# Performance work log

Hardware: AMD Instinct MI355X
Metric: run time of the kernel (lower is better)

## Reference

```python
import jax, jax.numpy as jnp
import numpy as np

N, E, G = 10000, 160000, 64
NODE_DIM, HID = 128, 256


def _edge_conv(x, src, dst, w1, b1, w2, b2):
    # gather endpoints: x_i = target features, x_j = source features (PyG source_to_target)
    x_i = x[dst]                              # [E, C]
    x_j = x[src]                              # [E, C]
    m = jnp.concatenate([x_i, x_j - x_i], axis=-1)  # [E, 2C]
    m = jax.nn.relu(m @ w1 + b1) @ w2 + b2          # [E, H]
    out = jax.ops.segment_max(m, dst, num_segments=N)  # scatter-max per target node
    return out  # nodes with no in-edges get -inf; subsequent relu maps them to 0 (matches PyG fill 0 + relu)


def setup_inputs() -> dict:
    key = jax.random.key(0)
    ks = jax.random.split(key, 20)
    x = jax.random.normal(ks[0], (N, NODE_DIM), dtype=jnp.float32)
    edge_index = jax.random.randint(ks[1], (2, E), 0, N)
    batch = jnp.sort(jax.random.randint(ks[2], (N,), 0, G))
    s = 0.05
    inp = {"x": x, "edge_index": edge_index, "batch": batch}
    dims = [(2 * NODE_DIM, HID), (2 * HID, HID), (2 * HID, HID)]
    for li, (din, dout) in enumerate(dims):
        inp[f"c{li}_w1"] = jax.random.normal(ks[3 + 4 * li], (din, dout), jnp.float32) * s
        inp[f"c{li}_b1"] = jnp.zeros((dout,), jnp.float32)
        inp[f"c{li}_w2"] = jax.random.normal(ks[4 + 4 * li], (dout, dout), jnp.float32) * s
        inp[f"c{li}_b2"] = jnp.zeros((dout,), jnp.float32)
    inp["cl_w1"] = jax.random.normal(ks[15], (2 * HID, HID), jnp.float32) * s
    inp["cl_b1"] = jnp.zeros((HID,), jnp.float32)
    inp["cl_w2"] = jax.random.normal(ks[16], (HID, 64), jnp.float32) * s
    inp["cl_b2"] = jnp.zeros((64,), jnp.float32)
    inp["cl_w3"] = jax.random.normal(ks[17], (64, 1), jnp.float32) * s
    inp["cl_b3"] = jnp.zeros((1,), jnp.float32)
    return inp


def reference(x, edge_index, batch,
              c0_w1, c0_b1, c0_w2, c0_b2,
              c1_w1, c1_b1, c1_w2, c1_b2,
              c2_w1, c2_b1, c2_w2, c2_b2,
              cl_w1, cl_b1, cl_w2, cl_b2, cl_w3, cl_b3):
    src, dst = edge_index[0], edge_index[1]
    for (w1, b1, w2, b2) in [(c0_w1, c0_b1, c0_w2, c0_b2),
                             (c1_w1, c1_b1, c1_w2, c1_b2),
                             (c2_w1, c2_b1, c2_w2, c2_b2)]:
        x = jax.nn.relu(_edge_conv(x, src, dst, w1, b1, w2, b2))
    # global mean / max pool per graph
    sums = jax.ops.segment_sum(x, batch, num_segments=G)
    counts = jax.ops.segment_sum(jnp.ones((x.shape[0], 1), x.dtype), batch, num_segments=G)
    x_mean = sums / jnp.maximum(counts, 1.0)
    x_max = jax.ops.segment_max(x, batch, num_segments=G)
    x_max = jnp.where(counts > 0, x_max, 0.0)
    h = jnp.concatenate([x_mean, x_max], axis=1)  # [G, 2H]
    h = jax.nn.relu(h @ cl_w1 + cl_b1)            # dropout is eval-mode identity
    h = jax.nn.relu(h @ cl_w2 + cl_b2)
    out = (h @ cl_w3 + cl_b3).squeeze(-1)         # [G]
    return out
```

## Files before the change

kernel.cpp:

```cpp
#include <hip/hip_runtime.h>


#define NN 10000
#define NE 160000
#define NG 64
#define NP 10048
#define EB 64
#define TPB 5
#define NBLK 500

typedef __attribute__((ext_vector_type(8))) _Float16 f16x8;
typedef __attribute__((ext_vector_type(4))) _Float16 f16x4;
typedef __attribute__((ext_vector_type(4))) float f32x4;

#define LGKM_BARRIER() asm volatile("s_waitcnt lgkmcnt(0)\n\ts_barrier" ::: "memory")

__global__ void hist_kernel(const int* __restrict__ dstI, int* __restrict__ hist) {
    int i = blockIdx.x * blockDim.x + threadIdx.x;
    if (i < NE) atomicAdd(&hist[dstI[i]], 1);
}

__global__ void scan_kernel(const int* __restrict__ hist, int* __restrict__ cursor) {
    __shared__ int sums[256];
    const int t = threadIdx.x;
    const int per = (NN + 255) / 256;
    const int lo = t * per, hi = (lo + per < NN) ? lo + per : NN;
    int s = 0;
    for (int i = lo; i < hi; ++i) s += hist[i];
    sums[t] = s;
    __syncthreads();
    for (int ofs = 1; ofs < 256; ofs <<= 1) {
        int add = (t >= ofs) ? sums[t - ofs] : 0;
        __syncthreads();
        sums[t] += add;
        __syncthreads();
    }
    int run = sums[t] - s;
    for (int i = lo; i < hi; ++i) {
        int h = hist[i];
        cursor[i] = run;
        run += h;
    }
}

__global__ void scatter_kernel(const int* __restrict__ srcI, const int* __restrict__ dstI,
                               int* __restrict__ cursor,
                               int* __restrict__ se2, int* __restrict__ de2) {
    int i = blockIdx.x * blockDim.x + threadIdx.x;
    if (i < NE) {
        int d = dstI[i];
        int p = atomicAdd(&cursor[d], 1);
        se2[p] = srcI[i];
        de2[p] = d;
    }
}

__global__ void prep_weights(const float* __restrict__ w1, const float* __restrict__ w2, int C,
                             _Float16* __restrict__ WcT, _Float16* __restrict__ w2T) {
    int total1 = 512 * C;
    int total = total1 + 256 * 256;
    for (int i = blockIdx.x * blockDim.x + threadIdx.x; i < total; i += gridDim.x * blockDim.x) {
        if (i < total1) {
            int n = i / C, k = i - n * C;
            float v = (n < 256) ? (w1[k * 256 + n] - w1[(C + k) * 256 + n])
                                : w1[(C + k) * 256 + (n - 256)];
            WcT[n * C + k] = (_Float16)v;
        } else {
            int j = i - total1;
            int n = j >> 8, k = j & 255;
            w2T[n * 256 + k] = (_Float16)w2[k * 256 + n];
        }
    }
}

template <int C>
__global__ __launch_bounds__(256, 2) void node_gemm(
    const float* __restrict__ xf, const _Float16* __restrict__ WT,
    const float* __restrict__ b1, _Float16* __restrict__ Afh, _Float16* __restrict__ Bh) {
    const int wave = threadIdx.x >> 6, lane = threadIdx.x & 63;
    const int lrow = lane & 15, lk = (lane >> 4) * 8;
    const int r0 = blockIdx.x * 64;
    const int c0 = blockIdx.y * 256 + wave * 64;

    f32x4 acc[4][4] = {};
#pragma unroll
    for (int kk = 0; kk < C; kk += 32) {
        f16x8 ah[4];
#pragma unroll
        for (int m = 0; m < 4; ++m) {
            int rc = r0 + m * 16 + lrow;
            if (rc > NN - 1) rc = NN - 1;
            const float* xp = xf + (size_t)rc * C + kk + lk;
            const float4 v0 = *(const float4*)(xp);
            const float4 v1 = *(const float4*)(xp + 4);
            f16x8 a;
            a[0] = (_Float16)v0.x; a[1] = (_Float16)v0.y;
            a[2] = (_Float16)v0.z; a[3] = (_Float16)v0.w;
            a[4] = (_Float16)v1.x; a[5] = (_Float16)v1.y;
            a[6] = (_Float16)v1.z; a[7] = (_Float16)v1.w;
            ah[m] = a;
        }
#pragma unroll
        for (int t = 0; t < 4; ++t) {
            f16x8 bh = *(const f16x8*)(WT + (size_t)(c0 + t * 16 + lrow) * C + kk + lk);
#pragma unroll
            for (int m = 0; m < 4; ++m)
                acc[m][t] = __builtin_amdgcn_mfma_f32_16x16x32_f16(ah[m], bh, acc[m][t], 0, 0, 0);
        }
    }
    if (blockIdx.y == 0) {
#pragma unroll
        for (int t = 0; t < 4; ++t) {
            const int col = c0 + t * 16 + lrow;
            const float bias = b1[col];
#pragma unroll
            for (int m = 0; m < 4; ++m)
#pragma unroll
                for (int j = 0; j < 4; ++j) {
                    const int row = r0 + m * 16 + (lane >> 4) * 4 + j;
                    Afh[(size_t)row * 256 + col] = (_Float16)(acc[m][t][j] + bias);
                }
        }
    } else {
#pragma unroll
        for (int t = 0; t < 4; ++t) {
            const int col = c0 - 256 + t * 16 + lrow;
#pragma unroll
            for (int m = 0; m < 4; ++m)
#pragma unroll
                for (int j = 0; j < 4; ++j) {
                    const int row = r0 + m * 16 + (lane >> 4) * 4 + j;
                    Bh[(size_t)row * 256 + col] = (_Float16)acc[m][t][j];
                }
        }
    }
}

__global__ __launch_bounds__(512, 2) void edge_gemm(
    const _Float16* __restrict__ Afh, const _Float16* __restrict__ Bh,
    const int* __restrict__ se2, const int* __restrict__ de2,
    const _Float16* __restrict__ w2T,
    const float* __restrict__ b2, float* __restrict__ y) {
    __shared__ _Float16 hh[2 * EB * 256];
    const int tid = threadIdx.x;
    const int wave = tid >> 6, lane = tid & 63;
    const int lrow = lane & 15, lk = (lane >> 4) * 8;

    const int orig = blockIdx.x;
    const int xcd = orig & 7, pos = orig >> 3;
    const int qq = NBLK >> 3, rr = NBLK & 7;
    const int bid = (xcd < rr ? xcd * (qq + 1) : rr * (qq + 1) + (xcd - rr) * qq) + pos;
    const int t0 = bid * TPB;

    const _Float16* wbase = w2T + (size_t)(wave * 32 + lrow) * 256 + lk;

    f16x4 av[8], bv[8];

    auto stage_issue = [&](int tile) {
        int se[8], de[8];
#pragma unroll
        for (int i = 0; i < 8; ++i) {
            const int e = tile * EB + wave * 8 + i;
            se[i] = se2[e];
            de[i] = de2[e];
        }
#pragma unroll
        for (int i = 0; i < 8; ++i) {
            bv[i] = *(const f16x4*)(Bh + (size_t)se[i] * 256 + lane * 4);
            av[i] = *(const f16x4*)(Afh + (size_t)de[i] * 256 + lane * 4);
        }
    };
    auto stage_write = [&](int buf) {
#pragma unroll
        for (int i = 0; i < 8; ++i) {
            const int el = wave * 8 + i;
            const int row = ((el >> 2) & 3) * 16 + (el >> 4) * 4 + (el & 3);
            f16x4 h = av[i] + bv[i];
#pragma unroll
            for (int k = 0; k < 4; ++k) h[k] = h[k] > (_Float16)0.f ? h[k] : (_Float16)0.f;
            *(f16x4*)(&hh[buf * (EB * 256) + ((row * 256 + lane * 4) ^ ((row & 15) << 3))]) = h;
        }
    };

    stage_issue(t0);
    stage_write(0);
    LGKM_BARRIER();

    for (int tt = 0; tt < TPB; ++tt) {
        const int tile = t0 + tt;
        const int hbase = (tt & 1) * (EB * 256);

        if (tt + 1 < TPB) stage_issue(tile + 1);

        f32x4 acc[4][2] = {};
#pragma unroll
        for (int q = 0; q < 8; ++q) {
            f16x8 bh0 = *(const f16x8*)(wbase + q * 32);
            f16x8 bh1 = *(const f16x8*)(wbase + 16 * 256 + q * 32);
            f16x8 ah[4];
#pragma unroll
            for (int m = 0; m < 4; ++m) {
                const int row = m * 16 + lrow;
                const int idx = (row * 256 + q * 32 + lk) ^ ((row & 15) << 3);
                ah[m] = *(const f16x8*)(&hh[hbase + idx]);
            }
#pragma unroll
            for (int m = 0; m < 4; ++m) {
                acc[m][0] = __builtin_amdgcn_mfma_f32_16x16x32_f16(ah[m], bh0, acc[m][0], 0, 0, 0);
                acc[m][1] = __builtin_amdgcn_mfma_f32_16x16x32_f16(ah[m], bh1, acc[m][1], 0, 0, 0);
            }
        }

        if (tt + 1 < TPB) stage_write((tt + 1) & 1);
        LGKM_BARRIER();

        {
            const int g = lane >> 4;
            const int e0 = tile * EB;
            int d[16];
#pragma unroll
            for (int k = 0; k < 16; ++k) d[k] = de2[e0 + g * 16 + k];
#pragma unroll
            for (int t = 0; t < 2; ++t) {
                const int col = wave * 32 + t * 16 + lrow;
                const float bias = b2[col];
                float run = acc[0][t][0];
                int dp = d[0];
#pragma unroll
                for (int k = 1; k < 16; ++k) {
                    const float v = acc[k >> 2][t][k & 3];
                    if (d[k] == dp) {
                        run = fmaxf(run, v);
                    } else {
                        const float o = run + bias;
                        if (o > 0.f) atomicMax((int*)(y + (size_t)dp * 256 + col), __float_as_int(o));
                        run = v;
                        dp = d[k];
                    }
                }
                const float o = run + bias;
                if (o > 0.f) atomicMax((int*)(y + (size_t)dp * 256 + col), __float_as_int(o));
            }
        }
    }
}

__global__ void pool_kernel(const float* __restrict__ y, const int* __restrict__ batch,
                            float* __restrict__ pooled) {
    const int g = blockIdx.x;
    __shared__ int slo, shi;
    __shared__ float ssum[4][256];
    __shared__ float smax[4][256];
    const int c = threadIdx.x, ry = threadIdx.y;
    if (c == 0 && ry == 0) {
        int lo = 0, hi = NN;
        while (lo < hi) { int m = (lo + hi) >> 1; if (batch[m] < g) lo = m + 1; else hi = m; }
        slo = lo;
        int lo2 = lo, hi2 = NN;
        while (lo2 < hi2) { int m = (lo2 + hi2) >> 1; if (batch[m] < g + 1) lo2 = m + 1; else hi2 = m; }
        shi = lo2;
    }
    __syncthreads();
    const int lo = slo, hi = shi;
    float s = 0.f, mx = 0.f;
    for (int n = lo + ry; n < hi; n += 4) {
        const float v = y[(size_t)n * 256 + c];
        s += v;
        mx = fmaxf(mx, v);
    }
    ssum[ry][c] = s;
    smax[ry][c] = mx;
    __syncthreads();
    if (ry == 0) {
        const float st = (ssum[0][c] + ssum[1][c]) + (ssum[2][c] + ssum[3][c]);
        const float mt = fmaxf(fmaxf(smax[0][c], smax[1][c]), fmaxf(smax[2][c], smax[3][c]));
        const int cnt = hi - lo;
        pooled[g * 512 + c] = cnt ? st / (float)cnt : 0.f;
        pooled[g * 512 + 256 + c] = cnt ? mt : 0.f;
    }
}

__global__ void classifier(const float* __restrict__ pooled,
                           const float* __restrict__ w1, const float* __restrict__ b1,
                           const float* __restrict__ w2, const float* __restrict__ b2,
                           const float* __restrict__ w3, const float* __restrict__ b3,
                           float* __restrict__ out) {
    const int g = blockIdx.x;
    __shared__ float ph[512];
    __shared__ float o1[256];
    __shared__ float o2[64];
    const int t = threadIdx.x;
    ph[t] = pooled[g * 512 + t];
    ph[t + 256] = pooled[g * 512 + 256 + t];
    __syncthreads();
    float s = 0.f;
    for (int k = 0; k < 512; ++k) s += ph[k] * w1[k * 256 + t];
    o1[t] = fmaxf(s + b1[t], 0.f);
    __syncthreads();
    if (t < 64) {
        float s2 = 0.f;
        for (int k = 0; k < 256; ++k) s2 += o1[k] * w2[k * 64 + t];
        o2[t] = fmaxf(s2 + b2[t], 0.f);
    }
    __syncthreads();
    if (t < 64) {
        float v = o2[t] * w3[t];
        for (int off = 32; off; off >>= 1) v += __shfl_down(v, off);
        if (t == 0) out[g] = v + b3[0];
    }
}

extern "C" void kernel_launch(void* const* d_in, const int* in_sizes, int n_in,
                              void* d_out, int out_size, void* d_ws, size_t ws_size,
                              hipStream_t stream) {
    (void)in_sizes; (void)n_in; (void)out_size; (void)ws_size;
    const float* x0 = (const float*)d_in[0];
    const int* eidx = (const int*)d_in[1];
    const int* batch = (const int*)d_in[2];
    const int* srcI = eidx;
    const int* dstI = eidx + NE;

    char* ws = (char*)d_ws;
    size_t off = 0;
    auto alloc = [&](size_t bytes) -> void* {
        void* p = ws + off;
        off += (bytes + 255) & ~(size_t)255;
        return p;
    };
    _Float16* Afh = (_Float16*)alloc((size_t)NP * 256 * 2);
    _Float16* Bh  = (_Float16*)alloc((size_t)NP * 256 * 2);
    float* y  = (float*)alloc((size_t)NP * 256 * 4);
    _Float16* WcT = (_Float16*)alloc(512 * 256 * 2);
    _Float16* w2T = (_Float16*)alloc(256 * 256 * 2);
    float* pooled = (float*)alloc(64 * 512 * 4);
    int* hist = (int*)alloc(NN * 4);
    int* se2 = (int*)alloc(NE * 4);
    int* de2 = (int*)alloc(NE * 4);

    const float* lw[3][4] = {
        {(const float*)d_in[3],  (const float*)d_in[4],  (const float*)d_in[5],  (const float*)d_in[6]},
        {(const float*)d_in[7],  (const float*)d_in[8],  (const float*)d_in[9],  (const float*)d_in[10]},
        {(const float*)d_in[11], (const float*)d_in[12], (const float*)d_in[13], (const float*)d_in[14]},
    };

    hipMemsetAsync(hist, 0, NN * 4, stream);
    hist_kernel<<<dim3((NE + 255) / 256), dim3(256), 0, stream>>>(dstI, hist);
    scan_kernel<<<dim3(1), dim3(256), 0, stream>>>(hist, hist);
    scatter_kernel<<<dim3((NE + 255) / 256), dim3(256), 0, stream>>>(srcI, dstI, hist, se2, de2);

    for (int l = 0; l < 3; ++l) {
        const int C = (l == 0) ? 128 : 256;
        prep_weights<<<dim3(256), dim3(256), 0, stream>>>(lw[l][0], lw[l][2], C, WcT, w2T);
        if (C == 128)
            node_gemm<128><<<dim3(NP / 64, 2), dim3(256), 0, stream>>>(x0, WcT, lw[l][1], Afh, Bh);
        else
            node_gemm<256><<<dim3(NP / 64, 2), dim3(256), 0, stream>>>(y, WcT, lw[l][1], Afh, Bh);
        hipMemsetAsync(y, 0, (size_t)NP * 256 * 4, stream);
        edge_gemm<<<dim3(NBLK), dim3(512), 0, stream>>>(Afh, Bh, se2, de2, w2T, lw[l][3], y);
    }

    pool_kernel<<<dim3(NG), dim3(256, 4), 0, stream>>>(y, batch, pooled);
    classifier<<<dim3(NG), dim3(256), 0, stream>>>(pooled,
        (const float*)d_in[15], (const float*)d_in[16],
        (const float*)d_in[17], (const float*)d_in[18],
        (const float*)d_in[19], (const float*)d_in[20], (float*)d_out);
}
```

Measured before the change: 356.3 us.

## Pad per-destination edge segments to 16 so each window has one target

Edge lists sorted by destination are padded to multiples of 16 by repeating a source, and per-16-edge window metadata records the destination node and its position. The edge kernel then loads one target feature row per wave instead of one per edge. The segment max becomes a full reduction followed by two cross-lane shuffles. Windows that fully own a node's segment use plain stores instead of atomicMax. This removes the de2 index array and most atomics, but adds padded edge work (a larger grid, some blocks exiting early) and two extra preprocessing kernels.

```diff
diff --git a/kernel.cpp b/kernel.cpp
--- a/kernel.cpp
+++ b/kernel.cpp
@@ -7,7 +7,9 @@
 #define NP 10048
 #define EB 64
 #define TPB 5
-#define NBLK 500
+#define NBLK2 969
+#define CAPE (NBLK2 * TPB * 64)
+#define CAPW (CAPE / 16)
 
 typedef __attribute__((ext_vector_type(8))) _Float16 f16x8;
 typedef __attribute__((ext_vector_type(4))) _Float16 f16x4;
@@ -15,18 +17,26 @@
 
 #define LGKM_BARRIER() asm volatile("s_waitcnt lgkmcnt(0)\n\ts_barrier" ::: "memory")
 
+__global__ void init_pad(int* __restrict__ se3, unsigned* __restrict__ meta) {
+    const int i0 = blockIdx.x * blockDim.x + threadIdx.x;
+    const int stride = gridDim.x * blockDim.x;
+    for (int j = i0; j < CAPE; j += stride) se3[j] = 0;
+    for (int j = i0; j < CAPW; j += stride) meta[j] = ((unsigned)NN << 5) | 16u;
+}
+
 __global__ void hist_kernel(const int* __restrict__ dstI, int* __restrict__ hist) {
     int i = blockIdx.x * blockDim.x + threadIdx.x;
     if (i < NE) atomicAdd(&hist[dstI[i]], 1);
 }
 
-__global__ void scan_kernel(const int* __restrict__ hist, int* __restrict__ cursor) {
+__global__ void scan_kernel(const int* __restrict__ hist, int* __restrict__ pstart,
+                            int* __restrict__ cursor, int* __restrict__ einfo) {
     __shared__ int sums[256];
     const int t = threadIdx.x;
     const int per = (NN + 255) / 256;
     const int lo = t * per, hi = (lo + per < NN) ? lo + per : NN;
     int s = 0;
-    for (int i = lo; i < hi; ++i) s += hist[i];
+    for (int i = lo; i < hi; ++i) s += (hist[i] + 15) & ~15;
     sums[t] = s;
     __syncthreads();
     for (int ofs = 1; ofs < 256; ofs <<= 1) {
@@ -37,21 +47,38 @@
     }
     int run = sums[t] - s;
     for (int i = lo; i < hi; ++i) {
-        int h = hist[i];
+        const int p = (hist[i] + 15) & ~15;
+        pstart[i] = run;
         cursor[i] = run;
-        run += h;
-    }
+        run += p;
+    }
+    if (t == 255) einfo[0] = run;
 }
 
 __global__ void scatter_kernel(const int* __restrict__ srcI, const int* __restrict__ dstI,
-                               int* __restrict__ cursor,
-                               int* __restrict__ se2, int* __restrict__ de2) {
+                               int* __restrict__ cursor, int* __restrict__ se3) {
     int i = blockIdx.x * blockDim.x + threadIdx.x;
     if (i < NE) {
-        int d = dstI[i];
-        int p = atomicAdd(&cursor[d], 1);
-        se2[p] = srcI[i];
-        de2[p] = d;
+        int p = atomicAdd(&cursor[dstI[i]], 1);
+        se3[p] = srcI[i];
+    }
+}
+
+__global__ void fill_meta(const int* __restrict__ hist, const int* __restrict__ pstart,
+                          int* __restrict__ se3, unsigned* __restrict__ meta) {
+    const int i0 = blockIdx.x * blockDim.x + threadIdx.x;
+    for (int d = i0; d < NN; d += gridDim.x * blockDim.x) {
+        const int deg = hist[d];
+        if (deg == 0) continue;
+        const int st = pstart[d];
+        const int padded = (deg + 15) & ~15;
+        const int s0 = se3[st];
+        for (int i = deg; i < padded; ++i) se3[st + i] = s0;
+        const int nwin = padded >> 4;
+        const int w0 = st >> 4;
+        for (int j = 0; j < nwin; ++j)
+            meta[w0 + j] = ((unsigned)d << 5) | ((j == nwin - 1) ? 16u : 0u)
+                         | (unsigned)(j < 15 ? j : 15);
     }
 }
 
@@ -138,7 +165,8 @@
 
 __global__ __launch_bounds__(512, 2) void edge_gemm(
     const _Float16* __restrict__ Afh, const _Float16* __restrict__ Bh,
-    const int* __restrict__ se2, const int* __restrict__ de2,
+    const int* __restrict__ se3, const unsigned* __restrict__ meta,
+    const int* __restrict__ einfo,
     const _Float16* __restrict__ w2T,
     const float* __restrict__ b2, float* __restrict__ y) {
     __shared__ _Float16 hh[2 * EB * 256];
@@ -148,34 +176,38 @@
 
     const int orig = blockIdx.x;
     const int xcd = orig & 7, pos = orig >> 3;
-    const int qq = NBLK >> 3, rr = NBLK & 7;
+    const int qq = NBLK2 >> 3, rr = NBLK2 & 7;
     const int bid = (xcd < rr ? xcd * (qq + 1) : rr * (qq + 1) + (xcd - rr) * qq) + pos;
     const int t0 = bid * TPB;
 
+    const int ep = einfo[0];
+    const int tiles_real = (ep + 63) >> 6;
+    if (t0 >= tiles_real) return;
+    const int ntt = (tiles_real - t0 < TPB) ? (tiles_real - t0) : TPB;
+
     const _Float16* wbase = w2T + (size_t)(wave * 32 + lrow) * 256 + lk;
-
-    f16x4 av[8], bv[8];
+    const float bias0 = b2[wave * 32 + lrow];
+    const float bias1 = b2[wave * 32 + 16 + lrow];
+
+    f16x4 av, bv[8];
 
     auto stage_issue = [&](int tile) {
-        int se[8], de[8];
-#pragma unroll
-        for (int i = 0; i < 8; ++i) {
-            const int e = tile * EB + wave * 8 + i;
-            se[i] = se2[e];
-            de[i] = de2[e];
-        }
-#pragma unroll
-        for (int i = 0; i < 8; ++i) {
+        int dw = (int)(meta[tile * 4 + (wave >> 1)] >> 5);
+        if (dw >= NN) dw = 0;
+        int se[8];
+#pragma unroll
+        for (int i = 0; i < 8; ++i) se[i] = se3[tile * EB + wave * 8 + i];
+        av = *(const f16x4*)(Afh + (size_t)dw * 256 + lane * 4);
+#pragma unroll
+        for (int i = 0; i < 8; ++i)
             bv[i] = *(const f16x4*)(Bh + (size_t)se[i] * 256 + lane * 4);
-            av[i] = *(const f16x4*)(Afh + (size_t)de[i] * 256 + lane * 4);
-        }
     };
     auto stage_write = [&](int buf) {
 #pragma unroll
         for (int i = 0; i < 8; ++i) {
             const int el = wave * 8 + i;
             const int row = ((el >> 2) & 3) * 16 + (el >> 4) * 4 + (el & 3);
-            f16x4 h = av[i] + bv[i];
+            f16x4 h = av + bv[i];
 #pragma unroll
             for (int k = 0; k < 4; ++k) h[k] = h[k] > (_Float16)0.f ? h[k] : (_Float16)0.f;
             *(f16x4*)(&hh[buf * (EB * 256) + ((row * 256 + lane * 4) ^ ((row & 15) << 3))]) = h;
@@ -186,11 +218,11 @@
     stage_write(0);
     LGKM_BARRIER();
 
-    for (int tt = 0; tt < TPB; ++tt) {
+    for (int tt = 0; tt < ntt; ++tt) {
         const int tile = t0 + tt;
         const int hbase = (tt & 1) * (EB * 256);
 
-        if (tt + 1 < TPB) stage_issue(tile + 1);
+        if (tt + 1 < ntt) stage_issue(tile + 1);
 
         f32x4 acc[4][2] = {};
 #pragma unroll
@@ -211,35 +243,37 @@
             }
         }
 
-        if (tt + 1 < TPB) stage_write((tt + 1) & 1);
+        if (tt + 1 < ntt) stage_write((tt + 1) & 1);
         LGKM_BARRIER();
 
         {
             const int g = lane >> 4;
-            const int e0 = tile * EB;
-            int d[16];
-#pragma unroll
-            for (int k = 0; k < 16; ++k) d[k] = de2[e0 + g * 16 + k];
+            const unsigned mt = meta[tile * 4 + g];
+            const int d = (int)(mt >> 5);
+            const int lastw = (int)((mt >> 4) & 1u);
+            const int wbm = (int)(mt & 15u);
 #pragma unroll
             for (int t = 0; t < 2; ++t) {
+                const float bias = t ? bias1 : bias0;
                 const int col = wave * 32 + t * 16 + lrow;
-                const float bias = b2[col];
-                float run = acc[0][t][0];
-                int dp = d[0];
-#pragma unroll
-                for (int k = 1; k < 16; ++k) {
-                    const float v = acc[k >> 2][t][k & 3];
-                    if (d[k] == dp) {
-                        run = fmaxf(run, v);
-                    } else {
-                        const float o = run + bias;
-                        if (o > 0.f) atomicMax((int*)(y + (size_t)dp * 256 + col), __float_as_int(o));
-                        run = v;
-                        dp = d[k];
+                float v = acc[0][t][0];
+#pragma unroll
+                for (int k = 1; k < 16; ++k) v = fmaxf(v, acc[k >> 2][t][k & 3]);
+                float pv = __shfl(v, (lane - 16) & 63);
+                int pd = __shfl(d, (lane - 16) & 63);
+                if (g >= 1 && pd == d) v = fmaxf(v, pv);
+                float pv2 = __shfl(v, (lane - 32) & 63);
+                int pd2 = __shfl(d, (lane - 32) & 63);
+                if (g >= 2 && pd2 == d) v = fmaxf(v, pv2);
+                if (d < NN) {
+                    const float o = v + bias;
+                    if (lastw && wbm <= g) {
+                        y[(size_t)d * 256 + col] = fmaxf(o, 0.f);
+                    } else if ((lastw && wbm > g) || (!lastw && g == 3)) {
+                        if (o > 0.f)
+                            atomicMax((int*)(y + (size_t)d * 256 + col), __float_as_int(o));
                     }
                 }
-                const float o = run + bias;
-                if (o > 0.f) atomicMax((int*)(y + (size_t)dp * 256 + col), __float_as_int(o));
             }
         }
     }
@@ -333,9 +367,12 @@
     _Float16* WcT = (_Float16*)alloc(512 * 256 * 2);
     _Float16* w2T = (_Float16*)alloc(256 * 256 * 2);
     float* pooled = (float*)alloc(64 * 512 * 4);
-    int* hist = (int*)alloc(NN * 4);
-    int* se2 = (int*)alloc(NE * 4);
-    int* de2 = (int*)alloc(NE * 4);
+    int* hist   = (int*)alloc(NN * 4);
+    int* pstart = (int*)alloc(NN * 4);
+    int* cursor = (int*)alloc(NN * 4);
+    int* einfo  = (int*)alloc(256);
+    int* se3    = (int*)alloc((size_t)CAPE * 4);
+    unsigned* meta = (unsigned*)alloc((size_t)CAPW * 4);
 
     const float* lw[3][4] = {
         {(const float*)d_in[3],  (const float*)d_in[4],  (const float*)d_in[5],  (const float*)d_in[6]},
@@ -343,10 +380,12 @@
         {(const float*)d_in[11], (const float*)d_in[12], (const float*)d_in[13], (const float*)d_in[14]},
     };
 
+    init_pad<<<dim3(512), dim3(256), 0, stream>>>(se3, meta);
     hipMemsetAsync(hist, 0, NN * 4, stream);
     hist_kernel<<<dim3((NE + 255) / 256), dim3(256), 0, stream>>>(dstI, hist);
-    scan_kernel<<<dim3(1), dim3(256), 0, stream>>>(hist, hist);
-    scatter_kernel<<<dim3((NE + 255) / 256), dim3(256), 0, stream>>>(srcI, dstI, hist, se2, de2);
+    scan_kernel<<<dim3(1), dim3(256), 0, stream>>>(hist, pstart, cursor, einfo);
+    scatter_kernel<<<dim3((NE + 255) / 256), dim3(256), 0, stream>>>(srcI, dstI, cursor, se3);
+    fill_meta<<<dim3(40), dim3(256), 0, stream>>>(hist, pstart, se3, meta);
 
     for (int l = 0; l < 3; ++l) {
         const int C = (l == 0) ? 128 : 256;
@@ -356,7 +395,7 @@
         else
             node_gemm<256><<<dim3(NP / 64, 2), dim3(256), 0, stream>>>(y, WcT, lw[l][1], Afh, Bh);
         hipMemsetAsync(y, 0, (size_t)NP * 256 * 4, stream);
-        edge_gemm<<<dim3(NBLK), dim3(512), 0, stream>>>(Afh, Bh, se2, de2, w2T, lw[l][3], y);
+        edge_gemm<<<dim3(NBLK2), dim3(512), 0, stream>>>(Afh, Bh, se3, meta, einfo, w2T, lw[l][3], y);
     }
 
     pool_kernel<<<dim3(NG), dim3(256, 4), 0, stream>>>(y, batch, pooled);
```

New measurement: 400.6 us (median of 2 runs). +12.4%, slower.
